# Optimization experiments

Measured on AMD Instinct MI355X. Metric: run time of the kernel, lower is better.

## Reference

```python
import jax, jax.numpy as jnp
import numpy as np

P = 16      # patch size
D = 768     # d_model
H = 12      # heads
L = 12      # layers
F = 3072    # d_ff
NC = 1000   # num classes
B = 32
IMG = 224
S = (IMG // P) ** 2 + 1  # 197 tokens (CLS + patches)
EPS = 1e-5


def layernorm(x, s, b):
    m = jnp.mean(x, axis=-1, keepdims=True)
    v = jnp.var(x, axis=-1, keepdims=True)
    return (x - m) * jax.lax.rsqrt(v + EPS) * s + b


def setup_inputs() -> dict:
    key = jax.random.key(0)
    ks = jax.random.split(key, 16)
    sd = 0.02
    patch_dim = P * P * 3  # 768
    inp = {
        "img": jax.random.normal(ks[0], (B, 3, IMG, IMG), jnp.float32),
        "proj_w": jax.random.normal(ks[1], (patch_dim, D), jnp.float32) * sd,
        "proj_b": jnp.zeros((D,), jnp.float32),
        "cls_token": jax.random.normal(ks[2], (1, 1, D), jnp.float32) * sd,
        "pos_emb": jax.random.normal(ks[3], (1, S, D), jnp.float32) * sd,
        # stacked per-layer params [L, ...]
        "ln1_s": jnp.ones((L, D), jnp.float32),
        "ln1_b": jnp.zeros((L, D), jnp.float32),
        "wq": jax.random.normal(ks[4], (L, D, D), jnp.float32) * sd,
        "bq": jnp.zeros((L, D), jnp.float32),
        "wk": jax.random.normal(ks[5], (L, D, D), jnp.float32) * sd,
        "bk": jnp.zeros((L, D), jnp.float32),
        "wv": jax.random.normal(ks[6], (L, D, D), jnp.float32) * sd,
        "bv": jnp.zeros((L, D), jnp.float32),
        "wo": jax.random.normal(ks[7], (L, D, D), jnp.float32) * sd,
        "bo": jnp.zeros((L, D), jnp.float32),
        "ln2_s": jnp.ones((L, D), jnp.float32),
        "ln2_b": jnp.zeros((L, D), jnp.float32),
        "w1": jax.random.normal(ks[8], (L, D, F), jnp.float32) * sd,
        "b1": jnp.zeros((L, F), jnp.float32),
        "w2": jax.random.normal(ks[9], (L, F, D), jnp.float32) * sd,
        "b2": jnp.zeros((L, D), jnp.float32),
        "fnorm_s": jnp.ones((D,), jnp.float32),
        "fnorm_b": jnp.zeros((D,), jnp.float32),
        "head_w": jax.random.normal(ks[10], (D, NC), jnp.float32) * sd,
        "head_b": jnp.zeros((NC,), jnp.float32),
    }
    return inp


def vit_forward(img, proj_w, proj_b, cls_token, pos_emb, ln1_s, ln1_b,
                wq, bq, wk, bk, wv, bv, wo, bo, ln2_s, ln2_b,
                w1, b1, w2, b2, fnorm_s, fnorm_b, head_w, head_b):
    b = img.shape[0]
    g = IMG // P
    # rearrange 'b c (h ph) (w pw) -> b (h w) (ph pw c)'
    x = img.reshape(b, 3, g, P, g, P)
    x = x.transpose(0, 2, 4, 3, 5, 1).reshape(b, g * g, P * P * 3)
    x = x @ proj_w + proj_b                      # [b, 196, D]
    cls = jnp.broadcast_to(cls_token, (b, 1, D))
    x = jnp.concatenate([cls, x], axis=1)        # [b, 197, D]
    x = x + pos_emb                              # learnable positional encoding

    dk = D // H
    scale = 1.0 / jnp.sqrt(jnp.float32(dk))

    def layer(x, p):
        (l1s, l1b, Wq, Bq, Wk, Bk, Wv, Bv, Wo, Bo,
         l2s, l2b, W1, B1, W2, B2) = p
        # pre-norm self-attention with residual
        xn = layernorm(x, l1s, l1b)
        q = (xn @ Wq + Bq).reshape(b, S, H, dk)
        k = (xn @ Wk + Bk).reshape(b, S, H, dk)
        v = (xn @ Wv + Bv).reshape(b, S, H, dk)
        scores = jnp.einsum('bqhd,bkhd->bhqk', q, k) * scale
        attn = jax.nn.softmax(scores, axis=-1)
        ao = jnp.einsum('bhqk,bkhd->bqhd', attn, v).reshape(b, S, D)
        x = x + (ao @ Wo + Bo)
        # pre-norm FFN with residual
        xn = layernorm(x, l2s, l2b)
        h = jax.nn.gelu(xn @ W1 + B1, approximate=False)
        x = x + (h @ W2 + B2)
        return x, None

    params = (ln1_s, ln1_b, wq, bq, wk, bk, wv, bv, wo, bo,
              ln2_s, ln2_b, w1, b1, w2, b2)
    x, _ = jax.lax.scan(layer, x, params)
    x = layernorm(x, fnorm_s, fnorm_b)
    cls_out = x[:, 0, :]
    return cls_out @ head_w + head_b             # [b, num_classes]


def reference(img, proj_w, proj_b, cls_token, pos_emb, ln1_s, ln1_b,
              wq, bq, wk, bk, wv, bv, wo, bo, ln2_s, ln2_b,
              w1, b1, w2, b2, fnorm_s, fnorm_b, head_w, head_b):
    return vit_forward(img, proj_w, proj_b, cls_token, pos_emb, ln1_s, ln1_b,
                       wq, bq, wk, bk, wv, bv, wo, bo, ln2_s, ln2_b,
                       w1, b1, w2, b2, fnorm_s, fnorm_b, head_w, head_b)
```

## Files before the change

kernel.cpp:

```cpp
#include <hip/hip_runtime.h>
#include <stdint.h>

typedef __attribute__((ext_vector_type(4))) float  f32x4;
typedef __attribute__((ext_vector_type(8))) _Float16 f16x8;
typedef __attribute__((ext_vector_type(8))) unsigned short u16x8;

__device__ __forceinline__ unsigned short f2h(float f) {
    _Float16 h = (_Float16)f;
    union { _Float16 h; unsigned short u; } cv; cv.h = h; return cv.u;
}

__device__ __forceinline__ f32x4 mfma16(f16x8 a, f16x8 b, f32x4 c) {
    return __builtin_amdgcn_mfma_f32_16x16x32_f16(a, b, c, 0, 0, 0);
}

__device__ __forceinline__ void async16(const unsigned short* g, unsigned short* l) {
    __builtin_amdgcn_global_load_lds(
        (const __attribute__((address_space(1))) unsigned int*)g,
        (__attribute__((address_space(3))) unsigned int*)l,
        16, 0, 0);
}

template<int EPI>
__global__ __launch_bounds__(256, 3)
void gemm_k(const unsigned short* __restrict__ A, const unsigned short* __restrict__ Bw,
            int M, int K, int N,
            float* __restrict__ p0, unsigned short* __restrict__ p1,
            const float* __restrict__ p2, const float* __restrict__ p3,
            unsigned short* __restrict__ p4, unsigned short* __restrict__ p5)
{
    __shared__ unsigned short lA[2][64 * 64];
    __shared__ unsigned short lB[2][128 * 64];
    const int tid  = threadIdx.x;
    const int lane = tid & 63;
    const int wid  = tid >> 6;

    const int gx  = gridDim.x;
    const int nwg = gx * gridDim.y;
    const int lin = blockIdx.y * gx + blockIdx.x;
    const int q = nwg >> 3, r = nwg & 7;
    const int xcd = lin & 7, i = lin >> 3;
    const int wg  = (xcd < r ? xcd * (q + 1) : r * (q + 1) + (xcd - r) * q) + i;
    const int m0 = (wg / gx) * 64;
    const int n0 = (wg % gx) * 128;

    const int colBase = wid * 32;
    const int fr = lane & 15, fg = lane >> 4;

    f32x4 acc[4][2];
#pragma unroll
    for (int a = 0; a < 4; ++a)
#pragma unroll
        for (int b = 0; b < 2; ++b) acc[a][b] = (f32x4){0.f, 0.f, 0.f, 0.f};

    const int nk = K >> 6;

    auto stage = [&](int buf, int kt) {
        const int k0 = kt << 6;
#pragma unroll
        for (int h = 0; h < 6; ++h) {
            const int c = h * 256 + tid;
            const int wbase = h * 256 + wid * 64;
            if (c < 512) {
                const int row = c >> 3, kc = c & 7;
                const int gkc = kc ^ (row & 7);
                int ar = m0 + row; if (ar > M - 1) ar = M - 1;
                async16(A + (size_t)ar * K + k0 + gkc * 8,
                        &lA[buf][(size_t)wbase * 8]);
            } else {
                const int cb = c - 512;
                const int row = cb >> 3, kc = cb & 7;
                const int gkc = kc ^ (row & 7);
                async16(Bw + (size_t)(n0 + row) * K + k0 + gkc * 8,
                        &lB[buf][(size_t)(wbase - 512) * 8]);
            }
        }
    };

    stage(0, 0);
    for (int kt = 0; kt < nk; ++kt) {
        __syncthreads();
        if (kt + 1 < nk) stage((kt + 1) & 1, kt + 1);
        const int buf = kt & 1;
#pragma unroll
        for (int kk = 0; kk < 2; ++kk) {
            f16x8 af[4], bfv[2];
#pragma unroll
            for (int mi = 0; mi < 4; ++mi) {
                int row = mi * 16 + fr;
                int pc  = (kk * 4 + fg) ^ (row & 7);
                af[mi] = *(const f16x8*)(&lA[buf][row * 64 + pc * 8]);
            }
#pragma unroll
            for (int ni = 0; ni < 2; ++ni) {
                int row = colBase + ni * 16 + fr;
                int pc  = (kk * 4 + fg) ^ (row & 7);
                bfv[ni] = *(const f16x8*)(&lB[buf][row * 64 + pc * 8]);
            }
#pragma unroll
            for (int mi = 0; mi < 4; ++mi)
#pragma unroll
                for (int ni = 0; ni < 2; ++ni)
                    acc[mi][ni] = mfma16(af[mi], bfv[ni], acc[mi][ni]);
        }
    }

#pragma unroll
    for (int mi = 0; mi < 4; ++mi) {
#pragma unroll
        for (int ni = 0; ni < 2; ++ni) {
            const int col = n0 + colBase + ni * 16 + fr;
#pragma unroll
            for (int reg = 0; reg < 4; ++reg) {
                const int row = m0 + mi * 16 + fg * 4 + reg;
                if (row >= M) continue;
                const float v = acc[mi][ni][reg];
                if constexpr (EPI == 0) {
                    int mat = col / 768;
                    int w   = col - mat * 768;
                    int h   = w >> 6, d = w & 63;
                    int b   = row / 197, s = row - b * 197;
                    float val = v + p2[col];
                    if (mat == 2) {
                        p5[(((size_t)b * 12 + h) * 64 + d) * 208 + s] = f2h(val);
                    } else {
                        unsigned short* dst = (mat == 0) ? p1 : p4;
                        dst[(((size_t)b * 12 + h) * 197 + s) * 64 + d] = f2h(val);
                    }
                } else if constexpr (EPI == 1 || EPI == 3) {
                    size_t idx = (size_t)row * 768 + col;
                    p0[idx] = p0[idx] + v + p2[col];
                } else if constexpr (EPI == 2) {
                    float val = v + p2[col];
                    float g = 0.5f * val * (1.0f + erff(val * 0.70710678118654752f));
                    p1[(size_t)row * 3072 + col] = f2h(g);
                } else {
                    int b = row / 196, p = row - b * 196;
                    float val = v + p2[col] + p3[(size_t)(1 + p) * 768 + col];
                    p0[((size_t)(b * 197 + 1 + p)) * 768 + col] = val;
                }
            }
        }
    }
}

__global__ __launch_bounds__(256, 4)
void attn_k(const unsigned short* __restrict__ qb, const unsigned short* __restrict__ kb,
            const unsigned short* __restrict__ vt, unsigned short* __restrict__ ao)
{
    __shared__ float sc[32 * 210];
    __shared__ float rinv[32];

    const int qt = blockIdx.x;
    const int bh = blockIdx.y;
    const int b = bh / 12, h = bh - b * 12;
    const unsigned short* qh  = qb + (size_t)bh * 197 * 64;
    const unsigned short* kh  = kb + (size_t)bh * 197 * 64;
    const unsigned short* vth = vt + (size_t)bh * 64 * 208;
    const int tid = threadIdx.x, lane = tid & 63, wid = tid >> 6;
    const int fr = lane & 15, fg = lane >> 4;

    f16x8 qf[2][2];
#pragma unroll
    for (int mi = 0; mi < 2; ++mi)
#pragma unroll
        for (int kc = 0; kc < 2; ++kc) {
            int s = qt * 32 + mi * 16 + fr; if (s > 196) s = 196;
            qf[mi][kc] = *(const f16x8*)(qh + (size_t)s * 64 + kc * 32 + fg * 8);
        }

    for (int nt = wid; nt < 13; nt += 4) {
        f32x4 a0 = (f32x4){0.f,0.f,0.f,0.f}, a1 = a0;
        int rs = nt * 16 + fr; if (rs > 196) rs = 196;
#pragma unroll
        for (int kc = 0; kc < 2; ++kc) {
            f16x8 kf = *(const f16x8*)(kh + (size_t)rs * 64 + kc * 32 + fg * 8);
            a0 = mfma16(qf[0][kc], kf, a0);
            a1 = mfma16(qf[1][kc], kf, a1);
        }
        int ccol = nt * 16 + fr;
        bool valid = (ccol < 197);
#pragma unroll
        for (int reg = 0; reg < 4; ++reg) {
            int mr = fg * 4 + reg;
            sc[mr * 210 + ccol]        = valid ? a0[reg] * 0.125f : -1e30f;
            sc[(16 + mr) * 210 + ccol] = valid ? a1[reg] * 0.125f : -1e30f;
        }
    }
    __syncthreads();

    {
        int row = tid >> 3, j = tid & 7;
        float m = -1e30f;
        for (int c = j; c < 208; c += 8) m = fmaxf(m, sc[row * 210 + c]);
#pragma unroll
        for (int o = 1; o < 8; o <<= 1) m = fmaxf(m, __shfl_xor(m, o));
        float sum = 0.f;
        for (int c = j; c < 208; c += 8) {
            float e = __expf(sc[row * 210 + c] - m);
            sc[row * 210 + c] = e;
            sum += e;
        }
#pragma unroll
        for (int o = 1; o < 8; o <<= 1) sum += __shfl_xor(sum, o);
        if (j == 0) rinv[row] = 1.0f / sum;
    }
    __syncthreads();

    f32x4 o0 = (f32x4){0.f,0.f,0.f,0.f}, o1 = o0;
    const int dbase = wid * 16;
    for (int kt = 0; kt < 7; ++kt) {
        int kb8 = kt * 32 + fg * 8;
        f16x8 pa0, pa1, vf;
        if (kb8 >= 208) {
#pragma unroll
            for (int j = 0; j < 8; ++j) { pa0[j] = (_Float16)0.f; pa1[j] = (_Float16)0.f; vf[j] = (_Float16)0.f; }
        } else {
            const float* pr0 = &sc[fr * 210 + kb8];
            const float* pr1 = &sc[(16 + fr) * 210 + kb8];
#pragma unroll
            for (int j = 0; j < 8; ++j) { pa0[j] = (_Float16)pr0[j]; pa1[j] = (_Float16)pr1[j]; }
            vf = *(const f16x8*)(vth + (size_t)(dbase + fr) * 208 + kb8);
        }
        o0 = mfma16(pa0, vf, o0);
        o1 = mfma16(pa1, vf, o1);
    }
#pragma unroll
    for (int reg = 0; reg < 4; ++reg) {
        int mr0 = fg * 4 + reg, s0 = qt * 32 + mr0;
        if (s0 < 197)
            ao[((size_t)(b * 197 + s0)) * 768 + h * 64 + dbase + fr] = f2h(o0[reg] * rinv[mr0]);
        int mr1 = 16 + fg * 4 + reg, s1 = qt * 32 + mr1;
        if (s1 < 197)
            ao[((size_t)(b * 197 + s1)) * 768 + h * 64 + dbase + fr] = f2h(o1[reg] * rinv[mr1]);
    }
}

__global__ __launch_bounds__(256, 4)
void ln_k(const float* __restrict__ x, const float* __restrict__ gs,
          const float* __restrict__ gb, unsigned short* __restrict__ out)
{
    const int row = blockIdx.x;
    const int tid = threadIdx.x, lane = tid & 63, wid = tid >> 6;
    const float* xr = x + (size_t)row * 768;
    float v0 = xr[tid], v1 = xr[tid + 256], v2 = xr[tid + 512];
    float s = v0 + v1 + v2;
    float q = v0 * v0 + v1 * v1 + v2 * v2;
#pragma unroll
    for (int o = 1; o < 64; o <<= 1) { s += __shfl_xor(s, o); q += __shfl_xor(q, o); }
    __shared__ float ws[4], wq[4];
    if (lane == 0) { ws[wid] = s; wq[wid] = q; }
    __syncthreads();
    s = ws[0] + ws[1] + ws[2] + ws[3];
    q = wq[0] + wq[1] + wq[2] + wq[3];
    const float mean = s * (1.0f / 768.0f);
    const float rstd = rsqrtf(q * (1.0f / 768.0f) - mean * mean + 1e-5f);
    unsigned short* orow = out + (size_t)row * 768;
    orow[tid]       = f2h((v0 - mean) * rstd * gs[tid]       + gb[tid]);
    orow[tid + 256] = f2h((v1 - mean) * rstd * gs[tid + 256] + gb[tid + 256]);
    orow[tid + 512] = f2h((v2 - mean) * rstd * gs[tid + 512] + gb[tid + 512]);
}

__device__ __forceinline__ void convT_dev(const float* __restrict__ src,
                                          unsigned short* __restrict__ dst,
                                          int K, int N, int bx, int by)
{
    __shared__ float t[64][65];
    const int tid = threadIdx.x;
    const int n0 = bx * 64, k0 = by * 64;
    int r = tid >> 4, cq = tid & 15;
#pragma unroll
    for (int i = 0; i < 4; ++i) {
        f32x4 v = *(const f32x4*)(src + (size_t)(k0 + r + i * 16) * N + n0 + cq * 4);
        t[r + i * 16][cq * 4 + 0] = v.x;
        t[r + i * 16][cq * 4 + 1] = v.y;
        t[r + i * 16][cq * 4 + 2] = v.z;
        t[r + i * 16][cq * 4 + 3] = v.w;
    }
    __syncthreads();
    int nl = tid >> 2, kq = tid & 3;
    u16x8 o0, o1;
#pragma unroll
    for (int j = 0; j < 8; ++j) {
        o0[j] = f2h(t[kq * 16 + j][nl]);
        o1[j] = f2h(t[kq * 16 + 8 + j][nl]);
    }
    unsigned short* d = dst + (size_t)(n0 + nl) * K + k0 + kq * 16;
    *(u16x8*)(d)     = o0;
    *(u16x8*)(d + 8) = o1;
}

__global__ __launch_bounds__(256)
void convT_k(const float* __restrict__ src, unsigned short* __restrict__ dst, int K, int N)
{
    convT_dev(src, dst, K, N, blockIdx.x, blockIdx.y);
}

__global__ __launch_bounds__(256)
void prep_k(const float* __restrict__ wq, const float* __restrict__ wk,
            const float* __restrict__ wv, const float* __restrict__ wo,
            const float* __restrict__ w1, const float* __restrict__ w2,
            const float* __restrict__ bq, const float* __restrict__ bk,
            const float* __restrict__ bv,
            unsigned short* __restrict__ wqkvT, unsigned short* __restrict__ woT,
            unsigned short* __restrict__ w1T, unsigned short* __restrict__ w2T,
            float* __restrict__ bqkv)
{
    const int bid = blockIdx.x;
    if (bid == 1728) {
        for (int c = threadIdx.x; c < 2304; c += 256) {
            int m = c / 768, w = c - m * 768;
            bqkv[c] = (m == 0) ? bq[w] : (m == 1 ? bk[w] : bv[w]);
        }
        return;
    }
    const float* src; unsigned short* dst; int K, N, bx, by;
    if (bid < 576) {
        int mat = bid / 144, r = bid - mat * 144;
        K = 768; N = 768; bx = r % 12; by = r / 12;
        if (mat == 0)      { src = wq; dst = wqkvT; }
        else if (mat == 1) { src = wk; dst = wqkvT + 768ull * 768; }
        else if (mat == 2) { src = wv; dst = wqkvT + 1536ull * 768; }
        else               { src = wo; dst = woT; }
    } else if (bid < 1152) {
        int r = bid - 576; K = 768; N = 3072; bx = r % 48; by = r / 48;
        src = w1; dst = w1T;
    } else {
        int r = bid - 1152; K = 3072; N = 768; bx = r % 12; by = r / 12;
        src = w2; dst = w2T;
    }
    convT_dev(src, dst, K, N, bx, by);
}

__global__ __launch_bounds__(256)
void patch_k(const float* __restrict__ img, unsigned short* __restrict__ patches)
{
    const int t = blockIdx.x;
    const int pxy = threadIdx.x;
    const int b = t / 196, pi = t - b * 196;
    const int gy = pi / 14, gx = pi - gy * 14;
    const int py = pxy >> 4, px = pxy & 15;
    const int yy = gy * 16 + py, xx = gx * 16 + px;
    const float* base = img + ((size_t)b * 3 * 224 + yy) * 224 + xx;
    float c0 = base[0];
    float c1 = base[224 * 224];
    float c2 = base[2 * 224 * 224];
    unsigned short* d = patches + (size_t)t * 768 + pxy * 3;
    d[0] = f2h(c0); d[1] = f2h(c1); d[2] = f2h(c2);
}

__global__ void cls_k(const float* __restrict__ cls, const float* __restrict__ pos,
                      float* __restrict__ x)
{
    int c = blockIdx.x * 256 + threadIdx.x;
    int b = blockIdx.y;
    x[((size_t)b * 197) * 768 + c] = cls[c] + pos[c];
}

__global__ __launch_bounds__(256, 4)
void head_k(const float* __restrict__ x, const float* __restrict__ fs, const float* __restrict__ fb,
            const float* __restrict__ hw, const float* __restrict__ hb, float* __restrict__ out)
{
    __shared__ float xn[768];
    __shared__ float ws[4], wq_[4];
    const int b  = blockIdx.y;
    const int n0 = blockIdx.x * 125;
    const int tid = threadIdx.x, lane = tid & 63, wid = tid >> 6;
    const float* xr = x + (size_t)b * 197 * 768;
    float v0 = xr[tid], v1 = xr[tid + 256], v2 = xr[tid + 512];
    float s = v0 + v1 + v2, q = v0 * v0 + v1 * v1 + v2 * v2;
#pragma unroll
    for (int o = 1; o < 64; o <<= 1) { s += __shfl_xor(s, o); q += __shfl_xor(q, o); }
    if (lane == 0) { ws[wid] = s; wq_[wid] = q; }
    __syncthreads();
    s = ws[0] + ws[1] + ws[2] + ws[3];
    q = wq_[0] + wq_[1] + wq_[2] + wq_[3];
    float mean = s * (1.f / 768.f);
    float rstd = rsqrtf(q * (1.f / 768.f) - mean * mean + 1e-5f);
    xn[tid]       = (v0 - mean) * rstd * fs[tid]       + fb[tid];
    xn[tid + 256] = (v1 - mean) * rstd * fs[tid + 256] + fb[tid + 256];
    xn[tid + 512] = (v2 - mean) * rstd * fs[tid + 512] + fb[tid + 512];
    __syncthreads();

    const int nrel = tid >> 1, half = tid & 1;
    const int n = n0 + nrel;
    float acc = 0.f;
    if (nrel < 125) {
        const float* hp = hw + (size_t)(half * 384) * 1000 + n;
        const float* xp = xn + half * 384;
#pragma unroll 4
        for (int k = 0; k < 384; ++k) acc = fmaf(xp[k], hp[(size_t)k * 1000], acc);
    }
    acc += __shfl_xor(acc, 1);
    if (half == 0 && nrel < 125) out[(size_t)b * 1000 + n] = acc + hb[n];
}

extern "C" void kernel_launch(void* const* d_in, const int* in_sizes, int n_in,
                              void* d_out, int out_size, void* d_ws, size_t ws_size,
                              hipStream_t stream)
{
    (void)in_sizes; (void)n_in; (void)out_size; (void)ws_size;
    const float* img    = (const float*)d_in[0];
    const float* proj_w = (const float*)d_in[1];
    const float* proj_b = (const float*)d_in[2];
    const float* cls_t  = (const float*)d_in[3];
    const float* pos    = (const float*)d_in[4];
    const float* ln1_s  = (const float*)d_in[5];
    const float* ln1_b  = (const float*)d_in[6];
    const float* wq     = (const float*)d_in[7];
    const float* bq     = (const float*)d_in[8];
    const float* wk     = (const float*)d_in[9];
    const float* bk     = (const float*)d_in[10];
    const float* wv     = (const float*)d_in[11];
    const float* bv     = (const float*)d_in[12];
    const float* wo     = (const float*)d_in[13];
    const float* bo     = (const float*)d_in[14];
    const float* ln2_s  = (const float*)d_in[15];
    const float* ln2_b  = (const float*)d_in[16];
    const float* w1     = (const float*)d_in[17];
    const float* b1     = (const float*)d_in[18];
    const float* w2     = (const float*)d_in[19];
    const float* b2     = (const float*)d_in[20];
    const float* fs     = (const float*)d_in[21];
    const float* fb     = (const float*)d_in[22];
    const float* hw     = (const float*)d_in[23];
    const float* hb     = (const float*)d_in[24];

    char* ws = (char*)d_ws;
    size_t off = 0;
    auto alloc = [&](size_t bytes) -> char* {
        char* r = ws + off;
        off += (bytes + 255) & ~(size_t)255;
        return r;
    };
    unsigned short* wqkvT = (unsigned short*)alloc(2304ull * 768 * 2);
    unsigned short* woT   = (unsigned short*)alloc(768ull * 768 * 2);
    unsigned short* w1T   = (unsigned short*)alloc(3072ull * 768 * 2);
    unsigned short* w2T   = (unsigned short*)alloc(768ull * 3072 * 2);
    float*          bqkv  = (float*)alloc(2304 * 4);
    unsigned short* projT = (unsigned short*)alloc(768ull * 768 * 2);
    float*          x     = (float*)alloc(6304ull * 768 * 4);
    unsigned short* xn    = (unsigned short*)alloc(6304ull * 768 * 2);
    unsigned short* qbuf  = (unsigned short*)alloc(4841472ull * 2);
    unsigned short* kbuf  = (unsigned short*)alloc(4841472ull * 2);
    unsigned short* vbufT = (unsigned short*)alloc(384ull * 64 * 208 * 2);
    unsigned short* aob   = (unsigned short*)alloc(6304ull * 768 * 2);
    unsigned short* hbuf  = (unsigned short*)alloc(6304ull * 3072 * 2);
    unsigned short* patches = hbuf;

    convT_k<<<dim3(12, 12), 256, 0, stream>>>(proj_w, projT, 768, 768);
    patch_k<<<dim3(6272), 256, 0, stream>>>(img, patches);
    gemm_k<4><<<dim3(6, 98), 256, 0, stream>>>(patches, projT, 6272, 768, 768,
                                               x, nullptr, proj_b, pos, nullptr, nullptr);
    cls_k<<<dim3(3, 32), 256, 0, stream>>>(cls_t, pos, x);

    for (int l = 0; l < 12; ++l) {
        prep_k<<<dim3(1729), 256, 0, stream>>>(
            wq + (size_t)l * 768 * 768, wk + (size_t)l * 768 * 768,
            wv + (size_t)l * 768 * 768, wo + (size_t)l * 768 * 768,
            w1 + (size_t)l * 768 * 3072, w2 + (size_t)l * 3072 * 768,
            bq + l * 768, bk + l * 768, bv + l * 768,
            wqkvT, woT, w1T, w2T, bqkv);

        ln_k<<<dim3(6304), 256, 0, stream>>>(x, ln1_s + l * 768, ln1_b + l * 768, xn);
        gemm_k<0><<<dim3(18, 99), 256, 0, stream>>>(xn, wqkvT, 6304, 768, 2304,
                                                    nullptr, qbuf, bqkv, nullptr, kbuf, vbufT);
        attn_k<<<dim3(7, 384), 256, 0, stream>>>(qbuf, kbuf, vbufT, aob);
        gemm_k<1><<<dim3(6, 99), 256, 0, stream>>>(aob, woT, 6304, 768, 768,
                                                   x, nullptr, bo + l * 768, nullptr, nullptr, nullptr);
        ln_k<<<dim3(6304), 256, 0, stream>>>(x, ln2_s + l * 768, ln2_b + l * 768, xn);
        gemm_k<2><<<dim3(24, 99), 256, 0, stream>>>(xn, w1T, 6304, 768, 3072,
                                                    nullptr, hbuf, b1 + l * 3072, nullptr, nullptr, nullptr);
        gemm_k<3><<<dim3(6, 99), 256, 0, stream>>>(hbuf, w2T, 6304, 3072, 768,
                                                   x, nullptr, b2 + l * 768, nullptr, nullptr, nullptr);
    }

    head_k<<<dim3(8, 32), 256, 0, stream>>>(x, fs, fb, hw, hb, (float*)d_out);
}
```

Measured before the change: 3.376 ms.

## Add 256x256-tile 8-wave GEMM kernel for QKV and FFN1 projections

Introduces a new GEMM kernel with 256x256 output tiles, 512 threads, swizzled LDS layout, split-phase async global-to-LDS staging interleaved with MFMA quarters, and XCD-aware workgroup remapping. It replaces the 64x128-tile kernel for the QKV projection and the first FFN matmul, aiming for higher arithmetic intensity and less global traffic per output. The trade-off is far fewer workgroups (225 and 300) at one block per CU, which risks poor load balance and wave quantization on a large-CU device, plus heavy register pressure from 128 accumulator floats per thread.

```diff
diff --git a/kernel.cpp b/kernel.cpp
--- a/kernel.cpp
+++ b/kernel.cpp
@@ -19,6 +19,145 @@
         (const __attribute__((address_space(1))) unsigned int*)g,
         (__attribute__((address_space(3))) unsigned int*)l,
         16, 0, 0);
+}
+
+template<int EPI>
+__global__ __launch_bounds__(512, 1)
+void gemm256_k(const unsigned short* __restrict__ A,
+               const unsigned short* __restrict__ Bw,
+               int M, int K,
+               unsigned short* __restrict__ o1, const float* __restrict__ bias,
+               unsigned short* __restrict__ o4, unsigned short* __restrict__ o5)
+{
+    __shared__ unsigned short lds[65536];
+    const int tid = threadIdx.x, lane = tid & 63, w = tid >> 6;
+    const int wm = w >> 2, wn = w & 3;
+    const int fr = lane & 15, fg = lane >> 4;
+
+    const int gx  = gridDim.x;
+    const int nwg = gx * gridDim.y;
+    const int lin = blockIdx.y * gx + blockIdx.x;
+    const int q = nwg >> 3, r = nwg & 7;
+    const int xcd = lin & 7, bi = lin >> 3;
+    const int wg  = (xcd < r ? xcd * (q + 1) : r * (q + 1) + (xcd - r) * q) + bi;
+    const int m0 = (wg / gx) * 256;
+    const int n0 = (wg % gx) * 256;
+
+    f32x4 acc[8][4];
+#pragma unroll
+    for (int a = 0; a < 8; ++a)
+#pragma unroll
+        for (int b = 0; b < 4; ++b) acc[a][b] = (f32x4){0.f, 0.f, 0.f, 0.f};
+
+    const int NT = K >> 6;
+
+    auto stageH = [&](int d, int t, int rg) {
+#pragma unroll
+        for (int l = 0; l < 2; ++l) {
+            const int c   = l * 512 + tid;
+            const int row = c >> 3, kc = c & 7;
+            const int gkc = kc ^ (row & 7);
+            const unsigned short* src;
+            if (rg < 2) {
+                int ar = m0 + rg * 128 + row; if (ar > M - 1) ar = M - 1;
+                src = A + (size_t)ar * K + t * 64 + gkc * 8;
+            } else {
+                src = Bw + (size_t)(n0 + (rg - 2) * 128 + row) * K + t * 64 + gkc * 8;
+            }
+            async16(src, &lds[(size_t)((d * 4 + rg) * 1024 + l * 512 + w * 64) * 8]);
+        }
+    };
+
+    stageH(0, 0, 0); stageH(0, 0, 1); stageH(0, 0, 2); stageH(0, 0, 3);
+    stageH(1, 1, 2); stageH(1, 1, 3); stageH(1, 1, 0);
+    asm volatile("s_waitcnt vmcnt(6)" ::: "memory");
+    __builtin_amdgcn_s_barrier();
+
+    for (int t = 0; t < NT; ++t) {
+        const int d = t & 1, d1 = (t + 1) & 1;
+        f16x8 bfr[4][2];
+        f16x8 afr[2][2];
+#pragma unroll
+        for (int p = 0; p < 4; ++p) {
+            if (p == 0) {
+                const int breg = 2 + (wn >> 1);
+#pragma unroll
+                for (int nf = 0; nf < 4; ++nf)
+#pragma unroll
+                    for (int kk = 0; kk < 2; ++kk) {
+                        int rl = (wn & 1) * 64 + nf * 16 + fr;
+                        int pc = (kk * 4 + fg) ^ (rl & 7);
+                        bfr[nf][kk] = *(const f16x8*)(&lds[(size_t)((d * 4 + breg) * 1024 + rl * 8 + pc) * 8]);
+                    }
+            }
+            const int half = p >> 1;
+#pragma unroll
+            for (int j = 0; j < 2; ++j)
+#pragma unroll
+                for (int kk = 0; kk < 2; ++kk) {
+                    int rl = wm * 64 + ((2 * p + j) & 3) * 16 + fr;
+                    int pc = (kk * 4 + fg) ^ (rl & 7);
+                    afr[j][kk] = *(const f16x8*)(&lds[(size_t)((d * 4 + half) * 1024 + rl * 8 + pc) * 8]);
+                }
+            if (p == 0) {
+                if (t + 1 < NT) stageH(d1, t + 1, 1);
+            } else if (p == 1) {
+                if (t + 2 < NT) stageH(d, t + 2, 2);
+            } else if (p == 2) {
+                if (t + 2 < NT) stageH(d, t + 2, 3);
+            } else {
+                if (t + 2 < NT) {
+                    stageH(d, t + 2, 0);
+                    asm volatile("s_waitcnt vmcnt(6)" ::: "memory");
+                } else if (t + 1 < NT) {
+                    asm volatile("s_waitcnt vmcnt(0)" ::: "memory");
+                }
+            }
+            __builtin_amdgcn_s_barrier();
+            asm volatile("s_waitcnt lgkmcnt(0)" ::: "memory");
+            __builtin_amdgcn_s_setprio(1);
+#pragma unroll
+            for (int j = 0; j < 2; ++j)
+#pragma unroll
+                for (int nf = 0; nf < 4; ++nf)
+#pragma unroll
+                    for (int kk = 0; kk < 2; ++kk)
+                        acc[2 * p + j][nf] = mfma16(afr[j][kk], bfr[nf][kk], acc[2 * p + j][nf]);
+            __builtin_amdgcn_s_setprio(0);
+            __builtin_amdgcn_s_barrier();
+        }
+    }
+
+#pragma unroll
+    for (int mf = 0; mf < 8; ++mf) {
+#pragma unroll
+        for (int nf = 0; nf < 4; ++nf) {
+            const int col = n0 + wn * 64 + nf * 16 + fr;
+#pragma unroll
+            for (int reg = 0; reg < 4; ++reg) {
+                const int row = m0 + (mf < 4 ? 0 : 128) + wm * 64 + (mf & 3) * 16 + fg * 4 + reg;
+                if (row >= M) continue;
+                const float v = acc[mf][nf][reg];
+                if constexpr (EPI == 0) {
+                    int mat = col / 768;
+                    int ww  = col - mat * 768;
+                    int h   = ww >> 6, dd = ww & 63;
+                    int b   = row / 197, s = row - b * 197;
+                    float val = v + bias[col];
+                    if (mat == 2) {
+                        o5[(((size_t)b * 12 + h) * 64 + dd) * 208 + s] = f2h(val);
+                    } else {
+                        unsigned short* dst = (mat == 0) ? o1 : o4;
+                        dst[(((size_t)b * 12 + h) * 197 + s) * 64 + dd] = f2h(val);
+                    }
+                } else {
+                    float val = v + bias[col];
+                    float g = 0.5f * val * (1.0f + erff(val * 0.70710678118654752f));
+                    o1[(size_t)row * 3072 + col] = f2h(g);
+                }
+            }
+        }
+    }
 }
 
 template<int EPI>
@@ -115,19 +254,7 @@
                 const int row = m0 + mi * 16 + fg * 4 + reg;
                 if (row >= M) continue;
                 const float v = acc[mi][ni][reg];
-                if constexpr (EPI == 0) {
-                    int mat = col / 768;
-                    int w   = col - mat * 768;
-                    int h   = w >> 6, d = w & 63;
-                    int b   = row / 197, s = row - b * 197;
-                    float val = v + p2[col];
-                    if (mat == 2) {
-                        p5[(((size_t)b * 12 + h) * 64 + d) * 208 + s] = f2h(val);
-                    } else {
-                        unsigned short* dst = (mat == 0) ? p1 : p4;
-                        dst[(((size_t)b * 12 + h) * 197 + s) * 64 + d] = f2h(val);
-                    }
-                } else if constexpr (EPI == 1 || EPI == 3) {
+                if constexpr (EPI == 1 || EPI == 3) {
                     size_t idx = (size_t)row * 768 + col;
                     p0[idx] = p0[idx] + v + p2[col];
                 } else if constexpr (EPI == 2) {
@@ -142,6 +269,7 @@
             }
         }
     }
+    (void)p4; (void)p5;
 }
 
 __global__ __launch_bounds__(256, 4)
@@ -463,14 +591,14 @@
             wqkvT, woT, w1T, w2T, bqkv);
 
         ln_k<<<dim3(6304), 256, 0, stream>>>(x, ln1_s + l * 768, ln1_b + l * 768, xn);
-        gemm_k<0><<<dim3(18, 99), 256, 0, stream>>>(xn, wqkvT, 6304, 768, 2304,
-                                                    nullptr, qbuf, bqkv, nullptr, kbuf, vbufT);
+        gemm256_k<0><<<dim3(9, 25), 512, 0, stream>>>(xn, wqkvT, 6304, 768,
+                                                      qbuf, bqkv, kbuf, vbufT);
         attn_k<<<dim3(7, 384), 256, 0, stream>>>(qbuf, kbuf, vbufT, aob);
         gemm_k<1><<<dim3(6, 99), 256, 0, stream>>>(aob, woT, 6304, 768, 768,
                                                    x, nullptr, bo + l * 768, nullptr, nullptr, nullptr);
         ln_k<<<dim3(6304), 256, 0, stream>>>(x, ln2_s + l * 768, ln2_b + l * 768, xn);
-        gemm_k<2><<<dim3(24, 99), 256, 0, stream>>>(xn, w1T, 6304, 768, 3072,
-                                                    nullptr, hbuf, b1 + l * 3072, nullptr, nullptr, nullptr);
+        gemm256_k<2><<<dim3(12, 25), 512, 0, stream>>>(xn, w1T, 6304, 768,
+                                                       hbuf, b1 + l * 3072, nullptr, nullptr);
         gemm_k<3><<<dim3(6, 99), 256, 0, stream>>>(hbuf, w2T, 6304, 3072, 768,
                                                    x, nullptr, b2 + l * 768, nullptr, nullptr, nullptr);
     }
```

Measured after the change: 3.600 ms. +6.6%, slower.
